# Optimization experiments

Hardware: AMD Instinct MI355X
Metric: run time of the kernel (lower is better)

## Reference

```python
import jax, jax.numpy as jnp
import numpy as np

K = 3  # kernel size for all locally-connected layers

def lc2d(x, w, b, stride):
    """Locally connected 2d: per-output-location unshared weights.
    x: [B, C, H, W]; w: [1, O, C, Ho, Wo, K*K]; b: [1, O, Ho, Wo].
    Matches torch: x.unfold(2,K,s).unfold(3,K,s) -> [B,C,Ho,Wo,K,K] flattened
    to K*K, then (x[:,None]*w).sum([2,-1]) + b.
    """
    # patches: [B, C*K*K, Ho, Wo], feature order (c, kh, kw) == torch unfold order
    p = jax.lax.conv_general_dilated_patches(x, (K, K), (stride, stride), 'VALID')
    B, CKK, Ho, Wo = p.shape
    C = w.shape[2]
    p = p.reshape(B, C, K * K, Ho, Wo)
    out = jnp.einsum('bckhw,ochwk->bohw', p, w[0])
    return out + b

def setup_inputs() -> dict:
    key = jax.random.key(0)
    ks = jax.random.split(key, 11)
    s = 0.1
    return {
        'x':   jax.random.normal(ks[0], (8192, 1, 28, 28), dtype=jnp.float32),
        'w1':  jax.random.normal(ks[1], (1, 16, 1, 13, 13, 9), dtype=jnp.float32) * s,
        'b1':  jax.random.normal(ks[2], (1, 16, 13, 13), dtype=jnp.float32) * s,
        'w2':  jax.random.normal(ks[3], (1, 32, 16, 6, 6, 9), dtype=jnp.float32) * s,
        'b2':  jax.random.normal(ks[4], (1, 32, 6, 6), dtype=jnp.float32) * s,
        'w3':  jax.random.normal(ks[5], (1, 64, 32, 4, 4, 9), dtype=jnp.float32) * s,
        'b3':  jax.random.normal(ks[6], (1, 64, 4, 4), dtype=jnp.float32) * s,
        'fw1': jax.random.normal(ks[7], (512, 1024), dtype=jnp.float32) * 0.03,
        'fb1': jax.random.normal(ks[8], (512,), dtype=jnp.float32) * 0.03,
        'fw2': jax.random.normal(ks[9], (10, 512), dtype=jnp.float32) * 0.03,
        'fb2': jax.random.normal(ks[10], (10,), dtype=jnp.float32) * 0.03,
    }

def reference(x, w1, b1, w2, b2, w3, b3, fw1, fb1, fw2, fb2):
    h = jax.nn.relu(lc2d(x, w1, b1, stride=2))   # [B,16,13,13]
    h = jax.nn.relu(lc2d(h, w2, b2, stride=2))   # [B,32,6,6]
    h = lc2d(h, w3, b3, stride=1)                # [B,64,4,4]
    h = h.reshape(h.shape[0], -1)                # [B,1024]
    h = jax.nn.relu(h @ fw1.T + fb1)             # [B,512]
    return h @ fw2.T + fb2                       # [B,10]
```

## Files before the change

kernel.cpp:

```cpp
#include <hip/hip_runtime.h>

typedef __attribute__((ext_vector_type(8))) short short8v;
typedef __attribute__((ext_vector_type(4))) float f32x4;

static __device__ __forceinline__ unsigned short f2bf(float f) {
  union { float f; unsigned u; } v;
  v.f = f;
  const unsigned u = v.u;
  return (unsigned short)((u + 0x7FFF + ((u >> 16) & 1)) >> 16);
}
static __device__ __forceinline__ float bf2f(unsigned short s) {
  union { unsigned u; float f; } v;
  v.u = ((unsigned)s) << 16;
  return v.f;
}


__global__ __launch_bounds__(256) void k_lc1(const float* __restrict__ x,
                                             const float* __restrict__ w,
                                             const float* __restrict__ bias,
                                             unsigned short* __restrict__ out,
                                             int B) {
  __shared__ float Xs[64][89];
  __shared__ float Ws[16 * 117];
  __shared__ float Bs[208];
  const int tid = threadIdx.x;
  const int b0 = blockIdx.x * 64;
  const int ho = blockIdx.y;
  const int fbase = 2 * ho * 28;

  for (int i = tid; i < 16 * 117 / 3; i += 256) {
  }
  for (int i = tid; i < 1872; i += 256)
    Ws[i] = w[((size_t)(i / 117) * 169 + ho * 13) * 9 + (i % 117)];
  for (int i = tid; i < 208; i += 256)
    Bs[i] = bias[(i / 13) * 169 + ho * 13 + (i % 13)];

  for (int idx = tid; idx < 1344; idx += 256) {
    const int b = idx / 21, q = idx - b * 21;
    const float4 v =
        *(const float4*)&x[(size_t)(b0 + b) * 784 + fbase + q * 4];
    Xs[b][q * 4 + 0] = v.x;
    Xs[b][q * 4 + 1] = v.y;
    Xs[b][q * 4 + 2] = v.z;
    Xs[b][q * 4 + 3] = v.w;
  }
  __syncthreads();

  const int lane = tid & 63;
  const int o0 = (tid >> 6) * 4;
  float xv[3][27];
#pragma unroll
  for (int r = 0; r < 3; ++r)
#pragma unroll
    for (int col = 0; col < 27; ++col) xv[r][col] = Xs[lane][r * 28 + col];

  float acc[4][13];
#pragma unroll
  for (int oo = 0; oo < 4; ++oo)
#pragma unroll
    for (int wo = 0; wo < 13; ++wo) acc[oo][wo] = Bs[(o0 + oo) * 13 + wo];
#pragma unroll
  for (int oo = 0; oo < 4; ++oo)
#pragma unroll
    for (int wo = 0; wo < 13; ++wo) {
      const float* wp = &Ws[(o0 + oo) * 117 + wo * 9];
#pragma unroll
      for (int kh = 0; kh < 3; ++kh)
#pragma unroll
        for (int kw = 0; kw < 3; ++kw)
          acc[oo][wo] = fmaf(xv[kh][2 * wo + kw], wp[kh * 3 + kw], acc[oo][wo]);
    }
#pragma unroll
  for (int oo = 0; oo < 4; ++oo)
#pragma unroll
    for (int wo = 0; wo < 13; ++wo)
      out[(size_t)((o0 + oo) * 169 + ho * 13 + wo) * B + b0 + lane] =
          f2bf(fmaxf(acc[oo][wo], 0.f));
}

template <int O, int C, int NPOS, int Kpad>
__global__ void k_wmc(const float* __restrict__ w,
                      unsigned short* __restrict__ wm) {
  const int pos = blockIdx.x, o = blockIdx.y, k = threadIdx.x;
  float v = 0.f;
  if (k < C * 9) {
    const int c = k / 9, kk = k - c * 9;
    v = w[((size_t)(o * C + c) * NPOS + pos) * 9 + kk];
  }
  wm[((size_t)pos * O + o) * Kpad + k] = f2bf(v);
}

__global__ __launch_bounds__(256) void k_wbf(const float* __restrict__ w,
                                             unsigned short* __restrict__ o) {
  const int i = (blockIdx.x * 256 + threadIdx.x) * 8;
  const float4 a = *(const float4*)&w[i];
  const float4 b = *(const float4*)&w[i + 4];
  short8v r;
  r[0] = (short)f2bf(a.x); r[1] = (short)f2bf(a.y);
  r[2] = (short)f2bf(a.z); r[3] = (short)f2bf(a.w);
  r[4] = (short)f2bf(b.x); r[5] = (short)f2bf(b.y);
  r[6] = (short)f2bf(b.z); r[7] = (short)f2bf(b.w);
  *(short8v*)&o[i] = r;
}

template <int O, int K, int NPOS, int HWIN, int WIN, int WOD, int STR,
          bool RELU>
__global__ __launch_bounds__(256) void k_lcm(
    const unsigned short* __restrict__ X, const unsigned short* __restrict__ Wm,
    const float* __restrict__ bias, unsigned short* __restrict__ out, int B) {
  constexpr int NSTEP = (K + 31) / 32;
  constexpr int Kpad = NSTEP * 32;
  constexpr int NBT = (O == 64) ? 8 : 4;
  __shared__ short Wl[2][O * 40];
  __shared__ short Xl[2][5232];
  __shared__ int rowtab[Kpad];
  const int tid = threadIdx.x;
  const int b0 = blockIdx.x * 128;
  const int pos = blockIdx.y;
  const int ho = pos / WOD, wo = pos - ho * WOD;
  const int w = tid >> 6, l = tid & 63, m = l & 15, g = l >> 4;
  const int jw = (O == 64) ? w * 16 : (w & 1) * 16;
  const int boff = (O == 64) ? 0 : (w >> 1) * 64;

  for (int k = tid; k < Kpad; k += 256) {
    int r = 0;
    if (k < K) {
      const int c = k / 9, kk = k - c * 9;
      const int kh = kk / 3, kw = kk - kh * 3;
      r = c * HWIN + (ho * STR + kh) * WIN + (wo * STR + kw);
    }
    rowtab[k] = r;
  }
  __syncthreads();

  const unsigned short* wsrc = Wm + (size_t)pos * O * Kpad;
  const int wjj = tid >> 2, wko = (tid & 3) * 8;
  const bool wact = tid < O * 4;
  const int kp = tid >> 4, boct = (tid & 15) * 8;

  f32x4 acc[NBT];
#pragma unroll
  for (int bt = 0; bt < NBT; ++bt) acc[bt] = (f32x4){0.f, 0.f, 0.f, 0.f};

  short8v wreg, xa, xb;
  bool z0, z1;

  if (wact) wreg = *(const short8v*)&wsrc[(size_t)wjj * Kpad + wko];
  {
    const int k0 = 2 * kp;
    z0 = k0 >= K;
    z1 = k0 + 1 >= K;
    xa = *(const short8v*)(X + (size_t)rowtab[k0] * B + b0 + boct);
    xb = *(const short8v*)(X + (size_t)rowtab[k0 + 1] * B + b0 + boct);
  }
  if (wact) *(short8v*)&Wl[0][wjj * 40 + wko] = wreg;
  {
    unsigned* xl = (unsigned*)&Xl[0][0];
#pragma unroll
    for (int i = 0; i < 8; ++i) {
      const int b = boct + i;
      const unsigned lo = z0 ? 0u : (unsigned)(unsigned short)xa[i];
      const unsigned hi = z1 ? 0u : (unsigned)(unsigned short)xb[i];
      xl[b * 20 + (b >> 3) * 4 + kp] = lo | (hi << 16);
    }
  }
  __syncthreads();

  for (int t = 0; t < NSTEP; ++t) {
    const int cur = t & 1;
    if (t < NSTEP - 1) {
      const int kc = (t + 1) * 32;
      if (wact) wreg = *(const short8v*)&wsrc[(size_t)wjj * Kpad + kc + wko];
      const int k0 = kc + 2 * kp;
      z0 = k0 >= K;
      z1 = k0 + 1 >= K;
      xa = *(const short8v*)(X + (size_t)rowtab[k0] * B + b0 + boct);
      xb = *(const short8v*)(X + (size_t)rowtab[k0 + 1] * B + b0 + boct);
    }
    {
      const short8v aw = *(const short8v*)&Wl[cur][(jw + m) * 40 + g * 8];
      short8v bx[NBT];
#pragma unroll
      for (int bt = 0; bt < NBT; ++bt) {
        const int b = boff + bt * 16 + m;
        bx[bt] = *(const short8v*)&Xl[cur][b * 40 + (b >> 3) * 8 + g * 8];
      }
#pragma unroll
      for (int bt = 0; bt < NBT; ++bt)
        acc[bt] = __builtin_amdgcn_mfma_f32_16x16x32_bf16(aw, bx[bt], acc[bt],
                                                          0, 0, 0);
    }
    if (t < NSTEP - 1) {
      const int nxt = cur ^ 1;
      if (wact) *(short8v*)&Wl[nxt][wjj * 40 + wko] = wreg;
      unsigned* xl = (unsigned*)&Xl[nxt][0];
#pragma unroll
      for (int i = 0; i < 8; ++i) {
        const int b = boct + i;
        const unsigned lo = z0 ? 0u : (unsigned)(unsigned short)xa[i];
        const unsigned hi = z1 ? 0u : (unsigned)(unsigned short)xb[i];
        xl[b * 20 + (b >> 3) * 4 + kp] = lo | (hi << 16);
      }
    }
    __syncthreads();
  }

#pragma unroll
  for (int r = 0; r < 4; ++r) {
    const int o = jw + g * 4 + r;
    const int f = o * NPOS + pos;
    const float bz = bias[f];
#pragma unroll
    for (int bt = 0; bt < NBT; ++bt) {
      float v = acc[bt][r] + bz;
      if (RELU) v = fmaxf(v, 0.f);
      out[(size_t)f * B + b0 + boff + bt * 16 + m] = f2bf(v);
    }
  }
}

__global__ __launch_bounds__(256) void k_fc1m(
    const unsigned short* __restrict__ X,
    const unsigned short* __restrict__ Wbf, const float* __restrict__ fb1,
    unsigned short* __restrict__ out, int B) {
  __shared__ short Wl[2][5120];
  __shared__ short Xl[2][5232];
  const int tid = threadIdx.x;
  const int b0 = blockIdx.x * 128, j0 = blockIdx.y * 128;
  const int w = tid >> 6, l = tid & 63, m = l & 15, g = l >> 4;

  const int wj = tid >> 1, wkh = (tid & 1) * 16;
  const unsigned short* wsrc = Wbf + (size_t)(j0 + wj) * 1024 + wkh;
  const int kp = tid >> 4, boct = (tid & 15) * 8;
  const unsigned short* xsrc = X + (size_t)(2 * kp) * B + b0 + boct;

  f32x4 acc[2][8];
#pragma unroll
  for (int jt = 0; jt < 2; ++jt)
#pragma unroll
    for (int bt = 0; bt < 8; ++bt) acc[jt][bt] = (f32x4){0.f, 0.f, 0.f, 0.f};

  short8v wreg0, wreg1, xa, xb;

  wreg0 = *(const short8v*)(wsrc);
  wreg1 = *(const short8v*)(wsrc + 8);
  xa = *(const short8v*)(xsrc);
  xb = *(const short8v*)(xsrc + B);

  {
    *(short8v*)&Wl[0][wj * 40 + wkh] = wreg0;
    *(short8v*)&Wl[0][wj * 40 + wkh + 8] = wreg1;
    unsigned* xl = (unsigned*)&Xl[0][0];
#pragma unroll
    for (int i = 0; i < 8; ++i) {
      const int b = boct + i;
      xl[b * 20 + (b >> 3) * 4 + kp] = (unsigned)(unsigned short)xa[i] |
                                       ((unsigned)(unsigned short)xb[i] << 16);
    }
  }
  __syncthreads();

  for (int t = 0; t < 32; ++t) {
    const int cur = t & 1;
    if (t < 31) {
      const unsigned short* wp = wsrc + (t + 1) * 32;
      wreg0 = *(const short8v*)(wp);
      wreg1 = *(const short8v*)(wp + 8);
      const unsigned short* xp = xsrc + (size_t)(t + 1) * 32 * B;
      xa = *(const short8v*)(xp);
      xb = *(const short8v*)(xp + B);
    }
    {
      short8v aw[2], bx[8];
#pragma unroll
      for (int jt = 0; jt < 2; ++jt)
        aw[jt] = *(const short8v*)&Wl[cur][(w * 32 + jt * 16 + m) * 40 + g * 8];
#pragma unroll
      for (int bt = 0; bt < 8; ++bt) {
        const int b = bt * 16 + m;
        bx[bt] = *(const short8v*)&Xl[cur][b * 40 + (b >> 3) * 8 + g * 8];
      }
#pragma unroll
      for (int jt = 0; jt < 2; ++jt)
#pragma unroll
        for (int bt = 0; bt < 8; ++bt)
          acc[jt][bt] = __builtin_amdgcn_mfma_f32_16x16x32_bf16(
              aw[jt], bx[bt], acc[jt][bt], 0, 0, 0);
    }
    if (t < 31) {
      const int nxt = cur ^ 1;
      *(short8v*)&Wl[nxt][wj * 40 + wkh] = wreg0;
      *(short8v*)&Wl[nxt][wj * 40 + wkh + 8] = wreg1;
      unsigned* xl = (unsigned*)&Xl[nxt][0];
#pragma unroll
      for (int i = 0; i < 8; ++i) {
        const int b = boct + i;
        xl[b * 20 + (b >> 3) * 4 + kp] =
            (unsigned)(unsigned short)xa[i] |
            ((unsigned)(unsigned short)xb[i] << 16);
      }
    }
    __syncthreads();
  }

#pragma unroll
  for (int jt = 0; jt < 2; ++jt)
#pragma unroll
    for (int r = 0; r < 4; ++r) {
      const int j = j0 + w * 32 + jt * 16 + g * 4 + r;
      const float bj = fb1[j];
#pragma unroll
      for (int bt = 0; bt < 8; ++bt)
        out[(size_t)j * B + b0 + bt * 16 + m] =
            f2bf(fmaxf(acc[jt][bt][r] + bj, 0.f));
    }
}

__global__ __launch_bounds__(256) void k_fc2(
    const unsigned short* __restrict__ in, const float* __restrict__ fw2,
    const float* __restrict__ fb2, float* __restrict__ out, int B, int b0) {
  __shared__ float red[4][10][64];
  const int tx = threadIdx.x;
  const int b = blockIdx.x * 64 + tx;
  const int tyu = threadIdx.y;
  float acc[10];
#pragma unroll
  for (int i = 0; i < 10; ++i) acc[i] = 0.f;
  for (int kk = 0; kk < 128; ++kk) {
    const int k = tyu * 128 + kk;
    const float v = bf2f(in[(size_t)k * B + b]);
#pragma unroll
    for (int i = 0; i < 10; ++i) acc[i] = fmaf(v, fw2[i * 512 + k], acc[i]);
  }
#pragma unroll
  for (int i = 0; i < 10; ++i) red[tyu][i][tx] = acc[i];
  __syncthreads();
  if (threadIdx.y == 0) {
#pragma unroll
    for (int i = 0; i < 10; ++i) {
      const float s = fb2[i] + red[0][i][tx] + red[1][i][tx] + red[2][i][tx] +
                      red[3][i][tx];
      out[(size_t)(b0 + b) * 10 + i] = s;
    }
  }
}

extern "C" void kernel_launch(void* const* d_in, const int* in_sizes, int n_in,
                              void* d_out, int out_size, void* d_ws,
                              size_t ws_size, hipStream_t stream) {
  const float* x   = (const float*)d_in[0];
  const float* w1  = (const float*)d_in[1];
  const float* b1  = (const float*)d_in[2];
  const float* w2  = (const float*)d_in[3];
  const float* b2  = (const float*)d_in[4];
  const float* w3  = (const float*)d_in[5];
  const float* b3  = (const float*)d_in[6];
  const float* fw1 = (const float*)d_in[7];
  const float* fb1 = (const float*)d_in[8];
  const float* fw2 = (const float*)d_in[9];
  const float* fb2 = (const float*)d_in[10];
  float* out = (float*)d_out;

  const int B = in_sizes[0] / 784;

  const size_t nWm2 = (size_t)36 * 32 * 160 / 2;
  const size_t nWm3 = (size_t)16 * 64 * 288 / 2;
  const size_t nWbf = (size_t)512 * 1024 / 2;
  unsigned short* Wm2 = (unsigned short*)d_ws;
  unsigned short* Wm3 = (unsigned short*)((float*)d_ws + nWm2);
  unsigned short* Wbf = (unsigned short*)((float*)d_ws + nWm2 + nWm3);
  unsigned short* hbase = (unsigned short*)((float*)d_ws + nWm2 + nWm3 + nWbf);
  const size_t ws_rem = ws_size - (nWm2 + nWm3 + nWbf) * sizeof(float);

  const size_t per_elem = (size_t)(2704 + 1152 + 1024 + 512) * 2;
  int Bc = B;
  while ((size_t)Bc * per_elem > ws_rem && Bc > 512) Bc >>= 1;
  const int nch = B / Bc;

  unsigned short* H1 = hbase;
  unsigned short* H2 = H1 + (size_t)2704 * Bc;
  unsigned short* H3 = H2 + (size_t)1152 * Bc;
  unsigned short* H4 = H3 + (size_t)1024 * Bc;

  k_wmc<32, 16, 36, 160><<<dim3(36, 32), 160, 0, stream>>>(w2, Wm2);
  k_wmc<64, 32, 16, 288><<<dim3(16, 64), 288, 0, stream>>>(w3, Wm3);
  k_wbf<<<dim3(256), 256, 0, stream>>>(fw1, Wbf);

  for (int ch = 0; ch < nch; ++ch) {
    const float* xc = x + (size_t)ch * Bc * 784;
    const int b0 = ch * Bc;

    k_lc1<<<dim3(Bc / 64, 13), 256, 0, stream>>>(xc, w1, b1, H1, Bc);
    k_lcm<32, 144, 36, 169, 13, 6, 2, true>
        <<<dim3(Bc / 128, 36), 256, 0, stream>>>(H1, Wm2, b2, H2, Bc);
    k_lcm<64, 288, 16, 36, 6, 4, 1, false>
        <<<dim3(Bc / 128, 16), 256, 0, stream>>>(H2, Wm3, b3, H3, Bc);
    k_fc1m<<<dim3(Bc / 128, 4), 256, 0, stream>>>(H3, Wbf, fb1, H4, Bc);
    k_fc2<<<dim3(Bc / 64), dim3(64, 4), 0, stream>>>(H4, fw2, fb2, out, Bc,
                                                     b0);
  }
}
```

Before: 128.6 us.

## Rewrite first locally-connected layer as bf16 MFMA with pre-packed weights

```diff
diff --git a/kernel.cpp b/kernel.cpp
--- a/kernel.cpp
+++ b/kernel.cpp
@@ -16,67 +16,76 @@
 }
 
 
-__global__ __launch_bounds__(256) void k_lc1(const float* __restrict__ x,
-                                             const float* __restrict__ w,
-                                             const float* __restrict__ bias,
-                                             unsigned short* __restrict__ out,
-                                             int B) {
-  __shared__ float Xs[64][89];
-  __shared__ float Ws[16 * 117];
+__global__ void k_wm1(const float* __restrict__ w,
+                      unsigned short* __restrict__ wm) {
+  const int pos = blockIdx.x, o = blockIdx.y, k = threadIdx.x;
+  const float v = (k < 9) ? w[((size_t)o * 169 + pos) * 9 + k] : 0.f;
+  wm[((size_t)pos * 16 + o) * 32 + k] = f2bf(v);
+}
+
+__global__ __launch_bounds__(256) void k_lc1m(
+    const float* __restrict__ x, const unsigned short* __restrict__ Wm1,
+    const float* __restrict__ bias, unsigned short* __restrict__ out, int B) {
+  __shared__ unsigned short Xl[109 * 130];
+  __shared__ unsigned short Wl[13 * 16 * 40];
   __shared__ float Bs[208];
   const int tid = threadIdx.x;
-  const int b0 = blockIdx.x * 64;
+  const int b0 = blockIdx.x * 128;
   const int ho = blockIdx.y;
+  const int wv = tid >> 6, l = tid & 63, m = l & 15, g = l >> 4;
+
+  unsigned* xl32 = (unsigned*)Xl;
+  for (int i = tid; i < 25 * 65; i += 256) xl32[84 * 65 + i] = 0;
   const int fbase = 2 * ho * 28;
-
-  for (int i = tid; i < 16 * 117 / 3; i += 256) {
-  }
-  for (int i = tid; i < 1872; i += 256)
-    Ws[i] = w[((size_t)(i / 117) * 169 + ho * 13) * 9 + (i % 117)];
-  for (int i = tid; i < 208; i += 256)
-    Bs[i] = bias[(i / 13) * 169 + ho * 13 + (i % 13)];
-
-  for (int idx = tid; idx < 1344; idx += 256) {
+  for (int idx = tid; idx < 2688; idx += 256) {
     const int b = idx / 21, q = idx - b * 21;
     const float4 v =
         *(const float4*)&x[(size_t)(b0 + b) * 784 + fbase + q * 4];
-    Xs[b][q * 4 + 0] = v.x;
-    Xs[b][q * 4 + 1] = v.y;
-    Xs[b][q * 4 + 2] = v.z;
-    Xs[b][q * 4 + 3] = v.w;
-  }
+    const int e = q * 4;
+    Xl[(e + 0) * 130 + b] = f2bf(v.x);
+    Xl[(e + 1) * 130 + b] = f2bf(v.y);
+    Xl[(e + 2) * 130 + b] = f2bf(v.z);
+    Xl[(e + 3) * 130 + b] = f2bf(v.w);
+  }
+  for (int idx = tid; idx < 832; idx += 256) {
+    const int wo = idx >> 6, rem = idx & 63;
+    const int o = rem >> 2, s = rem & 3;
+    *(short8v*)&Wl[(wo * 16 + o) * 40 + s * 8] =
+        *(const short8v*)&Wm1[((size_t)(ho * 13 + wo) * 16 + o) * 32 + s * 8];
+  }
+  for (int i = tid; i < 208; i += 256)
+    Bs[i] = bias[(i / 13) * 169 + ho * 13 + (i % 13)];
   __syncthreads();
 
-  const int lane = tid & 63;
-  const int o0 = (tid >> 6) * 4;
-  float xv[3][27];
-#pragma unroll
-  for (int r = 0; r < 3; ++r)
-#pragma unroll
-    for (int col = 0; col < 27; ++col) xv[r][col] = Xs[lane][r * 28 + col];
-
-  float acc[4][13];
-#pragma unroll
-  for (int oo = 0; oo < 4; ++oo)
-#pragma unroll
-    for (int wo = 0; wo < 13; ++wo) acc[oo][wo] = Bs[(o0 + oo) * 13 + wo];
-#pragma unroll
-  for (int oo = 0; oo < 4; ++oo)
-#pragma unroll
-    for (int wo = 0; wo < 13; ++wo) {
-      const float* wp = &Ws[(o0 + oo) * 117 + wo * 9];
-#pragma unroll
-      for (int kh = 0; kh < 3; ++kh)
-#pragma unroll
-        for (int kw = 0; kw < 3; ++kw)
-          acc[oo][wo] = fmaf(xv[kh][2 * wo + kw], wp[kh * 3 + kw], acc[oo][wo]);
-    }
-#pragma unroll
-  for (int oo = 0; oo < 4; ++oo)
-#pragma unroll
-    for (int wo = 0; wo < 13; ++wo)
-      out[(size_t)((o0 + oo) * 169 + ho * 13 + wo) * B + b0 + lane] =
-          f2bf(fmaxf(acc[oo][wo], 0.f));
+  int rbase[8];
+#pragma unroll
+  for (int i = 0; i < 8; ++i) {
+    const int k = g * 8 + i;
+    const int kh = k / 3;
+    const int e = (k < 9) ? kh * 28 + (k - kh * 3) : 84;
+    rbase[i] = e * 130 + wv * 32 + m;
+  }
+
+#pragma unroll
+  for (int wo = 0; wo < 13; ++wo) {
+    const short8v aw = *(const short8v*)&Wl[(wo * 16 + m) * 40 + g * 8];
+#pragma unroll
+    for (int nt = 0; nt < 2; ++nt) {
+      short8v bx;
+#pragma unroll
+      for (int i = 0; i < 8; ++i)
+        bx[i] = (short)Xl[rbase[i] + wo * 260 + nt * 16];
+      const f32x4 acc = __builtin_amdgcn_mfma_f32_16x16x32_bf16(
+          aw, bx, (f32x4){0.f, 0.f, 0.f, 0.f}, 0, 0, 0);
+#pragma unroll
+      for (int r = 0; r < 4; ++r) {
+        const int o = g * 4 + r;
+        const float vv = fmaxf(acc[r] + Bs[o * 13 + wo], 0.f);
+        out[(size_t)(o * 169 + ho * 13 + wo) * B + b0 + wv * 32 + nt * 16 +
+            m] = f2bf(vv);
+      }
+    }
+  }
 }
 
 template <int O, int C, int NPOS, int Kpad>
@@ -364,14 +373,18 @@
 
   const int B = in_sizes[0] / 784;
 
+  const size_t nWm1 = (size_t)169 * 16 * 32 / 2;
   const size_t nWm2 = (size_t)36 * 32 * 160 / 2;
   const size_t nWm3 = (size_t)16 * 64 * 288 / 2;
   const size_t nWbf = (size_t)512 * 1024 / 2;
-  unsigned short* Wm2 = (unsigned short*)d_ws;
-  unsigned short* Wm3 = (unsigned short*)((float*)d_ws + nWm2);
-  unsigned short* Wbf = (unsigned short*)((float*)d_ws + nWm2 + nWm3);
-  unsigned short* hbase = (unsigned short*)((float*)d_ws + nWm2 + nWm3 + nWbf);
-  const size_t ws_rem = ws_size - (nWm2 + nWm3 + nWbf) * sizeof(float);
+  unsigned short* Wm1 = (unsigned short*)d_ws;
+  unsigned short* Wm2 = (unsigned short*)((float*)d_ws + nWm1);
+  unsigned short* Wm3 = (unsigned short*)((float*)d_ws + nWm1 + nWm2);
+  unsigned short* Wbf = (unsigned short*)((float*)d_ws + nWm1 + nWm2 + nWm3);
+  unsigned short* hbase =
+      (unsigned short*)((float*)d_ws + nWm1 + nWm2 + nWm3 + nWbf);
+  const size_t ws_rem =
+      ws_size - (nWm1 + nWm2 + nWm3 + nWbf) * sizeof(float);
 
   const size_t per_elem = (size_t)(2704 + 1152 + 1024 + 512) * 2;
   int Bc = B;
@@ -383,6 +396,7 @@
   unsigned short* H3 = H2 + (size_t)1152 * Bc;
   unsigned short* H4 = H3 + (size_t)1024 * Bc;
 
+  k_wm1<<<dim3(169, 16), 32, 0, stream>>>(w1, Wm1);
   k_wmc<32, 16, 36, 160><<<dim3(36, 32), 160, 0, stream>>>(w2, Wm2);
   k_wmc<64, 32, 16, 288><<<dim3(16, 64), 288, 0, stream>>>(w3, Wm3);
   k_wbf<<<dim3(256), 256, 0, stream>>>(fw1, Wbf);
@@ -391,7 +405,7 @@
     const float* xc = x + (size_t)ch * Bc * 784;
     const int b0 = ch * Bc;
 
-    k_lc1<<<dim3(Bc / 64, 13), 256, 0, stream>>>(xc, w1, b1, H1, Bc);
+    k_lc1m<<<dim3(Bc / 128, 13), 256, 0, stream>>>(xc, Wm1, b1, H1, Bc);
     k_lcm<32, 144, 36, 169, 13, 6, 2, true>
         <<<dim3(Bc / 128, 36), 256, 0, stream>>>(H1, Wm2, b2, H2, Bc);
     k_lcm<64, 288, 16, 36, 6, 4, 1, false>
```

Result: faster. 122.6 us (-4.7%).
